# Kernel tuning notes

Hardware: AMD Instinct MI355X
Metric: run time of the kernel (lower is better)

## Reference

```python
import jax, jax.numpy as jnp
import numpy as np

B, SQ, SK, H, NH = 2, 2048, 2048, 1024, 16
HD = H // NH  # 64


def setup_inputs() -> dict:
    key = jax.random.key(0)
    ks = jax.random.split(key, 12)
    s = 1.0 / np.sqrt(H)
    inp = {
        "query": jax.random.normal(ks[0], (B, SQ, H), jnp.float32),
        "key": jax.random.normal(ks[1], (B, SK, H), jnp.float32),
        "value": jax.random.normal(ks[2], (B, SK, H), jnp.float32),
        # lower-triangular causal mask [B, SQ, SK]; nonzero = attend
        "causal_mask": jnp.broadcast_to(
            jnp.tril(jnp.ones((SQ, SK), jnp.int32)), (B, SQ, SK)
        ),
        "Wq": jax.random.uniform(ks[3], (H, H), jnp.float32, -s, s),
        "bq": jnp.zeros((H,), jnp.float32),
        "Wk": jax.random.uniform(ks[4], (H, H), jnp.float32, -s, s),
        "bk": jnp.zeros((H,), jnp.float32),
        "Wv": jax.random.uniform(ks[5], (H, H), jnp.float32, -s, s),
        "bv": jnp.zeros((H,), jnp.float32),
        "Wo": jax.random.uniform(ks[6], (H, H), jnp.float32, -s, s),
        "bo": jnp.zeros((H,), jnp.float32),
        "ln_g": jnp.ones((H,), jnp.float32),
        "ln_b": jnp.zeros((H,), jnp.float32),
    }
    return inp


def _layer_norm(x, g, b, eps=1e-5):
    mu = jnp.mean(x, axis=-1, keepdims=True)
    var = jnp.var(x, axis=-1, keepdims=True)
    return (x - mu) * jax.lax.rsqrt(var + eps) * g + b


def reference(query, key, value, causal_mask, Wq, bq, Wk, bk, Wv, bv, Wo, bo, ln_g, ln_b):
    # projections (torch Linear: x @ W.T + b)
    q = (query @ Wq.T + bq).reshape(B, SQ, NH, HD)
    k = (key @ Wk.T + bk).reshape(B, SK, NH, HD)
    v = (value @ Wv.T + bv).reshape(B, SK, NH, HD)
    # scores [B, NH, SQ, SK]
    scores = jnp.einsum("bqhd,bkhd->bhqk", q, k) / np.sqrt(HD).astype(np.float32)
    scores = jnp.where(causal_mask[:, None, :, :] == 0, -jnp.inf, scores)
    attn = jax.nn.softmax(scores, axis=-1)
    # dropout is identity in eval mode
    out = jnp.einsum("bhqk,bkhd->bqhd", attn, v).reshape(B, SQ, H)
    out = out @ Wo.T + bo
    return _layer_norm(query + out, ln_g, ln_b)
```

## Files before the change

kernel.cpp:

```cpp
#include <hip/hip_runtime.h>
#include <hip/hip_bf16.h>

#define SQL 2048
#define SKL 2048
#define HH  1024
#define NHH 16
#define HDD 64
#define BB  2
#define MM  (BB*SQL)

typedef __attribute__((ext_vector_type(8))) short short8;
typedef __attribute__((ext_vector_type(4))) short short4v;
typedef __attribute__((ext_vector_type(4))) float f32x4;
typedef unsigned short u16;

__device__ inline u16 f2bf(float f) {
    unsigned int u = __float_as_uint(f);
    u += 0x7fffu + ((u >> 16) & 1u);
    return (u16)(u >> 16);
}

__device__ inline void gl_lds16(const void* g, void* l) {
    __builtin_amdgcn_global_load_lds(
        (const __attribute__((address_space(1))) unsigned int*)g,
        (__attribute__((address_space(3))) unsigned int*)l, 16, 0, 0);
}

__global__ __launch_bounds__(256) void cvt_all_kernel(
    const float* __restrict__ q, const float* __restrict__ k, const float* __restrict__ v,
    const float* __restrict__ wq, const float* __restrict__ wk,
    const float* __restrict__ wv, const float* __restrict__ wo,
    u16* __restrict__ xq, u16* __restrict__ xk, u16* __restrict__ xv,
    u16* __restrict__ wqb, u16* __restrict__ wkb, u16* __restrict__ wvb, u16* __restrict__ wob)
{
    int b = blockIdx.x;
    const float* src; u16* dst;
    if      (b < 4096)  { src = q;  dst = xq; }
    else if (b < 8192)  { src = k;  dst = xk;  b -= 4096; }
    else if (b < 12288) { src = v;  dst = xv;  b -= 8192; }
    else if (b < 13312) { src = wq; dst = wqb; b -= 12288; }
    else if (b < 14336) { src = wk; dst = wkb; b -= 13312; }
    else if (b < 15360) { src = wv; dst = wvb; b -= 14336; }
    else                { src = wo; dst = wob; b -= 15360; }
    int i = (b * 256 + threadIdx.x) * 4;
    float4 vv = *(const float4*)(src + i);
    ushort4 oo;
    oo.x = f2bf(vv.x); oo.y = f2bf(vv.y); oo.z = f2bf(vv.z); oo.w = f2bf(vv.w);
    *(ushort4*)(dst + i) = oo;
}

template<int MODE>
__global__ __launch_bounds__(256) void gemm_kernel(
    const u16* __restrict__ A0, const u16* __restrict__ A1,
    const u16* __restrict__ W0, const u16* __restrict__ W1,
    const float* __restrict__ bias0, const float* __restrict__ bias1,
    u16* __restrict__ o0, u16* __restrict__ o1,
    const float* __restrict__ resid, float* __restrict__ outf)
{
    const int z = blockIdx.z;
    const u16* A = (MODE == 0 && z == 1) ? A1 : A0;
    const u16* W = (MODE == 0 && z == 1) ? W1 : W0;
    const float* bias = (MODE == 0 && z == 1) ? bias1 : bias0;
    u16* outb = (MODE == 0 && z == 1) ? o1 : o0;
    const float scale = (MODE == 0 && z == 0) ? 0.125f * 1.4426950408889634f : 1.0f;

    __shared__ u16 lds_a[128 * 32];
    __shared__ u16 lds_b[128 * 32];

    const int t = threadIdx.x;
    const int lane = t & 63;
    const int quad = lane >> 4;
    const int lo = lane & 15;
    const int wv = t >> 6;
    const int wm = (wv >> 1) * 64, wn = (wv & 1) * 64;
    const int m0 = blockIdx.x * 128;
    const int n0 = blockIdx.y * 128;

    f32x4 acc[4][4];
#pragma unroll
    for (int i = 0; i < 4; i++)
#pragma unroll
        for (int j = 0; j < 4; j++) acc[i][j] = (f32x4){0.f, 0.f, 0.f, 0.f};

    const int sl0 = t, sl1 = 256 + t;
    const int r0 = sl0 >> 2, c0 = ((sl0 & 3) ^ ((r0 >> 1) & 3)) * 8;
    const int r1 = sl1 >> 2, c1 = ((sl1 & 3) ^ ((r1 >> 1) & 3)) * 8;

    for (int k0 = 0; k0 < HH; k0 += 32) {
        gl_lds16(A + (size_t)(m0 + r0) * HH + k0 + c0, &lds_a[sl0 * 8]);
        gl_lds16(A + (size_t)(m0 + r1) * HH + k0 + c1, &lds_a[sl1 * 8]);
        gl_lds16(W + (size_t)(n0 + r0) * HH + k0 + c0, &lds_b[sl0 * 8]);
        gl_lds16(W + (size_t)(n0 + r1) * HH + k0 + c1, &lds_b[sl1 * 8]);
        __syncthreads();
        short8 af[4], bf[4];
#pragma unroll
        for (int i = 0; i < 4; i++) {
            const int ra = wm + i * 16 + lo;
            const int rb = wn + i * 16 + lo;
            af[i] = *(const short8*)&lds_a[ra * 32 + ((quad ^ ((ra >> 1) & 3)) * 8)];
            bf[i] = *(const short8*)&lds_b[rb * 32 + ((quad ^ ((rb >> 1) & 3)) * 8)];
        }
#pragma unroll
        for (int i = 0; i < 4; i++)
#pragma unroll
            for (int j = 0; j < 4; j++) {
                if (MODE == 2)
                    acc[i][j] = __builtin_amdgcn_mfma_f32_16x16x32_bf16(bf[j], af[i], acc[i][j], 0, 0, 0);
                else
                    acc[i][j] = __builtin_amdgcn_mfma_f32_16x16x32_bf16(af[i], bf[j], acc[i][j], 0, 0, 0);
            }
        __syncthreads();
    }

#pragma unroll
    for (int i = 0; i < 4; i++) {
#pragma unroll
        for (int j = 0; j < 4; j++) {
#pragma unroll
            for (int r = 0; r < 4; r++) {
                if (MODE == 2) {
                    int dg  = n0 + wn + j * 16 + quad * 4 + r;
                    int tok = m0 + wm + i * 16 + lo;
                    float val = acc[i][j][r] + bias[dg];
                    int head = dg >> 6, d = dg & 63;
                    int bi = tok >> 11, s = tok & 2047;
                    outb[(((size_t)bi * NHH + head) * HDD + d) * SKL + s] = f2bf(val);
                } else {
                    int row = m0 + wm + i * 16 + quad * 4 + r;
                    int col = n0 + wn + j * 16 + lo;
                    float val = acc[i][j][r] + bias[col];
                    if (MODE == 0) {
                        val *= scale;
                        int bi = row >> 11, s = row & 2047;
                        int head = col >> 6, d = col & 63;
                        outb[(((size_t)bi * NHH + head) * SQL + s) * HDD + d] = f2bf(val);
                    } else {
                        val += resid[(size_t)row * HH + col];
                        outf[(size_t)row * HH + col] = val;
                    }
                }
            }
        }
    }
}

#define PSTR 72

__global__ __launch_bounds__(256) void attn_kernel(
    const u16* __restrict__ qb, const u16* __restrict__ kb, const u16* __restrict__ vtb,
    u16* __restrict__ attn_out)
{
    __shared__ u16 k_lds[64 * 64];
    __shared__ u16 vt_lds[64 * 64];
    __shared__ u16 p_lds[4 * 16 * PSTR];

    const int t = threadIdx.x;
    const int lane = t & 63;
    const int quad = lane >> 4;
    const int lo = lane & 15;
    const int w = t >> 6;
    const int qt = (SQL / 64 - 1) - (blockIdx.x >> 5);
    const int bh = blockIdx.x & 31;
    const int q0 = qt * 64;

    const u16* qbase = qb + ((size_t)bh * SQL + q0 + w * 16 + lo) * HDD + quad * 8;
    short8 qf0 = *(const short8*)qbase;
    short8 qf1 = *(const short8*)(qbase + 32);

    float m_s = -__builtin_inff(), l_s = 0.f;
    f32x4 o[4];
#pragma unroll
    for (int j = 0; j < 4; j++) o[j] = (f32x4){0.f, 0.f, 0.f, 0.f};

    const int sl0 = t, sl1 = 256 + t;
    const int r0 = sl0 >> 3, c0 = ((sl0 & 7) ^ (r0 & 7)) * 8;
    const int r1 = sl1 >> 3, c1 = ((sl1 & 7) ^ (r1 & 7)) * 8;
    const u16* kbh = kb + (size_t)bh * SKL * HDD;
    const u16* vbh = vtb + (size_t)bh * HDD * SKL;
    u16* ppriv = &p_lds[w * 16 * PSTR];

    for (int kt = 0; kt <= qt; kt++) {
        const int k0 = kt * 64;
        gl_lds16(kbh + (size_t)(k0 + r0) * HDD + c0, &k_lds[sl0 * 8]);
        gl_lds16(kbh + (size_t)(k0 + r1) * HDD + c1, &k_lds[sl1 * 8]);
        gl_lds16(vbh + (size_t)r0 * SKL + k0 + c0, &vt_lds[sl0 * 8]);
        gl_lds16(vbh + (size_t)r1 * SKL + k0 + c1, &vt_lds[sl1 * 8]);
        __syncthreads();

        f32x4 s[4];
#pragma unroll
        for (int nt = 0; nt < 4; nt++) {
            const int row = nt * 16 + lo;
            short8 kf0 = *(const short8*)&k_lds[row * 64 + ((quad ^ (row & 7)) * 8)];
            short8 kf1 = *(const short8*)&k_lds[row * 64 + (((4 + quad) ^ (row & 7)) * 8)];
            s[nt] = (f32x4){0.f, 0.f, 0.f, 0.f};
            s[nt] = __builtin_amdgcn_mfma_f32_16x16x32_bf16(kf0, qf0, s[nt], 0, 0, 0);
            s[nt] = __builtin_amdgcn_mfma_f32_16x16x32_bf16(kf1, qf1, s[nt], 0, 0, 0);
        }
        if (kt == qt) {
            const int ql = w * 16 + lo;
#pragma unroll
            for (int nt = 0; nt < 4; nt++)
#pragma unroll
                for (int r = 0; r < 4; r++)
                    if (nt * 16 + quad * 4 + r > ql) s[nt][r] = -__builtin_inff();
        }

        float mx = s[0][0];
#pragma unroll
        for (int nt = 0; nt < 4; nt++)
#pragma unroll
            for (int r = 0; r < 4; r++) mx = fmaxf(mx, s[nt][r]);
        mx = fmaxf(mx, __shfl_xor(mx, 16));
        mx = fmaxf(mx, __shfl_xor(mx, 32));
        float mnew = fmaxf(m_s, mx);
        float al = __builtin_amdgcn_exp2f(m_s - mnew);
        m_s = mnew;
        float rs = 0.f;
#pragma unroll
        for (int nt = 0; nt < 4; nt++)
#pragma unroll
            for (int r = 0; r < 4; r++) {
                s[nt][r] = __builtin_amdgcn_exp2f(s[nt][r] - m_s);
                rs += s[nt][r];
            }
        rs += __shfl_xor(rs, 16);
        rs += __shfl_xor(rs, 32);
        l_s = l_s * al + rs;

        float alr[4];
#pragma unroll
        for (int r = 0; r < 4; r++) alr[r] = __shfl(al, quad * 4 + r, 16);
#pragma unroll
        for (int nt = 0; nt < 4; nt++)
#pragma unroll
            for (int r = 0; r < 4; r++) o[nt][r] *= alr[r];

#pragma unroll
        for (int nt = 0; nt < 4; nt++) {
            short4v pk;
#pragma unroll
            for (int r = 0; r < 4; r++) pk[r] = (short)f2bf(s[nt][r]);
            *(short4v*)&ppriv[lo * PSTR + nt * 16 + quad * 4] = pk;
        }
        short8 pf0 = *(const short8*)&ppriv[lo * PSTR + quad * 8];
        short8 pf1 = *(const short8*)&ppriv[lo * PSTR + 32 + quad * 8];

#pragma unroll
        for (int nt = 0; nt < 4; nt++) {
            const int row = nt * 16 + lo;
            short8 vf0 = *(const short8*)&vt_lds[row * 64 + ((quad ^ (row & 7)) * 8)];
            short8 vf1 = *(const short8*)&vt_lds[row * 64 + (((4 + quad) ^ (row & 7)) * 8)];
            o[nt] = __builtin_amdgcn_mfma_f32_16x16x32_bf16(pf0, vf0, o[nt], 0, 0, 0);
            o[nt] = __builtin_amdgcn_mfma_f32_16x16x32_bf16(pf1, vf1, o[nt], 0, 0, 0);
        }
        __syncthreads();
    }

    const int b = bh >> 4, h = bh & 15;
    float inv[4];
#pragma unroll
    for (int r = 0; r < 4; r++) inv[r] = 1.0f / __shfl(l_s, quad * 4 + r, 16);
#pragma unroll
    for (int nt = 0; nt < 4; nt++)
#pragma unroll
        for (int r = 0; r < 4; r++) {
            int srow = q0 + w * 16 + quad * 4 + r;
            attn_out[((size_t)b * SQL + srow) * HH + h * HDD + nt * 16 + lo] =
                f2bf(o[nt][r] * inv[r]);
        }
}

__global__ __launch_bounds__(256) void ln_kernel(const float* __restrict__ x,
                                                 const float* __restrict__ g,
                                                 const float* __restrict__ bb,
                                                 float* __restrict__ out)
{
    const int row = blockIdx.x;
    const int t = threadIdx.x;
    const float* xr = x + (size_t)row * HH;
    float4 v = *(const float4*)(xr + t * 4);
    float s1 = v.x + v.y + v.z + v.w;
    float s2 = v.x * v.x + v.y * v.y + v.z * v.z + v.w * v.w;
#pragma unroll
    for (int off = 32; off; off >>= 1) { s1 += __shfl_xor(s1, off); s2 += __shfl_xor(s2, off); }
    __shared__ float red[8];
    if ((t & 63) == 0) { red[(t >> 6) * 2] = s1; red[(t >> 6) * 2 + 1] = s2; }
    __syncthreads();
    s1 = red[0] + red[2] + red[4] + red[6];
    s2 = red[1] + red[3] + red[5] + red[7];
    float mu = s1 * (1.0f / HH);
    float var = s2 * (1.0f / HH) - mu * mu;
    float rstd = rsqrtf(var + 1e-5f);
    float4 gg = *(const float4*)(g + t * 4);
    float4 b4 = *(const float4*)(bb + t * 4);
    float4 o;
    o.x = (v.x - mu) * rstd * gg.x + b4.x;
    o.y = (v.y - mu) * rstd * gg.y + b4.y;
    o.z = (v.z - mu) * rstd * gg.z + b4.z;
    o.w = (v.w - mu) * rstd * gg.w + b4.w;
    *(float4*)(out + (size_t)row * HH + t * 4) = o;
}

extern "C" void kernel_launch(void* const* d_in, const int* in_sizes, int n_in,
                              void* d_out, int out_size, void* d_ws, size_t ws_size,
                              hipStream_t stream)
{
    const float* query = (const float*)d_in[0];
    const float* key   = (const float*)d_in[1];
    const float* value = (const float*)d_in[2];
    const float* Wq = (const float*)d_in[4];
    const float* bq = (const float*)d_in[5];
    const float* Wk = (const float*)d_in[6];
    const float* bk = (const float*)d_in[7];
    const float* Wv = (const float*)d_in[8];
    const float* bv = (const float*)d_in[9];
    const float* Wo = (const float*)d_in[10];
    const float* bo = (const float*)d_in[11];
    const float* ln_g = (const float*)d_in[12];
    const float* ln_b = (const float*)d_in[13];
    float* out = (float*)d_out;

    char* wp = (char*)d_ws;
    auto alloc = [&](size_t bytes) { void* p = (void*)wp; wp += (bytes + 255) & ~(size_t)255; return p; };
    const int nW = HH * HH;
    const int nX = MM * HH;
    u16* wqb = (u16*)alloc((size_t)nW * 2);
    u16* wkb = (u16*)alloc((size_t)nW * 2);
    u16* wvb = (u16*)alloc((size_t)nW * 2);
    u16* wob = (u16*)alloc((size_t)nW * 2);
    u16* xq  = (u16*)alloc((size_t)nX * 2);
    u16* xk  = (u16*)alloc((size_t)nX * 2);
    u16* xv  = (u16*)alloc((size_t)nX * 2);
    u16* qbuf = (u16*)alloc((size_t)nX * 2);
    u16* kbuf = (u16*)alloc((size_t)nX * 2);
    u16* vbuf = (u16*)alloc((size_t)nX * 2);
    u16* attnb = (u16*)alloc((size_t)nX * 2);
    float* projf = (float*)alloc((size_t)nX * 4);

    cvt_all_kernel<<<16384, 256, 0, stream>>>(query, key, value, Wq, Wk, Wv, Wo,
                                              xq, xk, xv, wqb, wkb, wvb, wob);

    gemm_kernel<0><<<dim3(32, 8, 2), 256, 0, stream>>>(
        xq, xk, wqb, wkb, bq, bk, qbuf, kbuf, nullptr, nullptr);
    gemm_kernel<2><<<dim3(32, 8, 1), 256, 0, stream>>>(
        xv, xv, wvb, wvb, bv, bv, vbuf, vbuf, nullptr, nullptr);

    attn_kernel<<<1024, 256, 0, stream>>>(qbuf, kbuf, vbuf, attnb);

    gemm_kernel<1><<<dim3(32, 8, 1), 256, 0, stream>>>(
        attnb, attnb, wob, wob, bo, bo, nullptr, nullptr, query, projf);

    ln_kernel<<<MM, 256, 0, stream>>>(projf, ln_g, ln_b, out);
}
```

Baseline: 264.9 us.

## Merge QKV projections into one launch, add lazy softmax rescale and packed bf16 converts

The Q/K and V projection GEMMs now run as a single three-slice launch, and the output projection gets its own dedicated kernel. In attention, rescaling of the running max is skipped unless the max grows by more than 8 in log2 space, which saves exp and multiply work on most tiles. The bf16 conversions now use the hardware packed-convert instruction, and MFMA sections are wrapped in s_setprio. The lazy rescale keeps a stale max, which risks larger exponent values, and the merged launch puts a runtime z branch inside the GEMM inner loop.

```diff
diff --git a/kernel.cpp b/kernel.cpp
--- a/kernel.cpp
+++ b/kernel.cpp
@@ -10,7 +10,6 @@
 #define MM  (BB*SQL)
 
 typedef __attribute__((ext_vector_type(8))) short short8;
-typedef __attribute__((ext_vector_type(4))) short short4v;
 typedef __attribute__((ext_vector_type(4))) float f32x4;
 typedef unsigned short u16;
 
@@ -18,6 +17,12 @@
     unsigned int u = __float_as_uint(f);
     u += 0x7fffu + ((u >> 16) & 1u);
     return (u16)(u >> 16);
+}
+
+__device__ inline unsigned int cvt_pk_bf16(float lo, float hi) {
+    unsigned int r;
+    asm("v_cvt_pk_bf16_f32 %0, %1, %2" : "=v"(r) : "v"(lo), "v"(hi));
+    return r;
 }
 
 __device__ inline void gl_lds16(const void* g, void* l) {
@@ -44,25 +49,23 @@
     else                { src = wo; dst = wob; b -= 15360; }
     int i = (b * 256 + threadIdx.x) * 4;
     float4 vv = *(const float4*)(src + i);
-    ushort4 oo;
-    oo.x = f2bf(vv.x); oo.y = f2bf(vv.y); oo.z = f2bf(vv.z); oo.w = f2bf(vv.w);
-    *(ushort4*)(dst + i) = oo;
-}
-
-template<int MODE>
-__global__ __launch_bounds__(256) void gemm_kernel(
-    const u16* __restrict__ A0, const u16* __restrict__ A1,
-    const u16* __restrict__ W0, const u16* __restrict__ W1,
-    const float* __restrict__ bias0, const float* __restrict__ bias1,
-    u16* __restrict__ o0, u16* __restrict__ o1,
-    const float* __restrict__ resid, float* __restrict__ outf)
+    unsigned int d0 = cvt_pk_bf16(vv.x, vv.y);
+    unsigned int d1 = cvt_pk_bf16(vv.z, vv.w);
+    *(uint2*)(dst + i) = make_uint2(d0, d1);
+}
+
+__global__ __launch_bounds__(256) void proj_kernel(
+    const u16* __restrict__ xq, const u16* __restrict__ xk, const u16* __restrict__ xv,
+    const u16* __restrict__ wqb, const u16* __restrict__ wkb, const u16* __restrict__ wvb,
+    const float* __restrict__ bq, const float* __restrict__ bk, const float* __restrict__ bv,
+    u16* __restrict__ oq, u16* __restrict__ ok, u16* __restrict__ ov)
 {
     const int z = blockIdx.z;
-    const u16* A = (MODE == 0 && z == 1) ? A1 : A0;
-    const u16* W = (MODE == 0 && z == 1) ? W1 : W0;
-    const float* bias = (MODE == 0 && z == 1) ? bias1 : bias0;
-    u16* outb = (MODE == 0 && z == 1) ? o1 : o0;
-    const float scale = (MODE == 0 && z == 0) ? 0.125f * 1.4426950408889634f : 1.0f;
+    const u16* A      = (z == 0) ? xq  : (z == 1) ? xk  : xv;
+    const u16* W      = (z == 0) ? wqb : (z == 1) ? wkb : wvb;
+    const float* bias = (z == 0) ? bq  : (z == 1) ? bk  : bv;
+    u16* outb         = (z == 0) ? oq  : (z == 1) ? ok  : ov;
+    const float scale = (z == 0) ? 0.125f * 1.4426950408889634f : 1.0f;
 
     __shared__ u16 lds_a[128 * 32];
     __shared__ u16 lds_b[128 * 32];
@@ -100,15 +103,19 @@
             af[i] = *(const short8*)&lds_a[ra * 32 + ((quad ^ ((ra >> 1) & 3)) * 8)];
             bf[i] = *(const short8*)&lds_b[rb * 32 + ((quad ^ ((rb >> 1) & 3)) * 8)];
         }
-#pragma unroll
-        for (int i = 0; i < 4; i++)
-#pragma unroll
-            for (int j = 0; j < 4; j++) {
-                if (MODE == 2)
+        if (z == 2) {
+#pragma unroll
+            for (int i = 0; i < 4; i++)
+#pragma unroll
+                for (int j = 0; j < 4; j++)
                     acc[i][j] = __builtin_amdgcn_mfma_f32_16x16x32_bf16(bf[j], af[i], acc[i][j], 0, 0, 0);
-                else
+        } else {
+#pragma unroll
+            for (int i = 0; i < 4; i++)
+#pragma unroll
+                for (int j = 0; j < 4; j++)
                     acc[i][j] = __builtin_amdgcn_mfma_f32_16x16x32_bf16(af[i], bf[j], acc[i][j], 0, 0, 0);
-            }
+        }
         __syncthreads();
     }
 
@@ -118,7 +125,7 @@
         for (int j = 0; j < 4; j++) {
 #pragma unroll
             for (int r = 0; r < 4; r++) {
-                if (MODE == 2) {
+                if (z == 2) {
                     int dg  = n0 + wn + j * 16 + quad * 4 + r;
                     int tok = m0 + wm + i * 16 + lo;
                     float val = acc[i][j][r] + bias[dg];
@@ -128,20 +135,76 @@
                 } else {
                     int row = m0 + wm + i * 16 + quad * 4 + r;
                     int col = n0 + wn + j * 16 + lo;
-                    float val = acc[i][j][r] + bias[col];
-                    if (MODE == 0) {
-                        val *= scale;
-                        int bi = row >> 11, s = row & 2047;
-                        int head = col >> 6, d = col & 63;
-                        outb[(((size_t)bi * NHH + head) * SQL + s) * HDD + d] = f2bf(val);
-                    } else {
-                        val += resid[(size_t)row * HH + col];
-                        outf[(size_t)row * HH + col] = val;
-                    }
+                    float val = (acc[i][j][r] + bias[col]) * scale;
+                    int bi = row >> 11, s = row & 2047;
+                    int head = col >> 6, d = col & 63;
+                    outb[(((size_t)bi * NHH + head) * SQL + s) * HDD + d] = f2bf(val);
                 }
             }
         }
     }
+}
+
+__global__ __launch_bounds__(256) void outproj_kernel(
+    const u16* __restrict__ A, const u16* __restrict__ W,
+    const float* __restrict__ bias, const float* __restrict__ resid,
+    float* __restrict__ outf)
+{
+    __shared__ u16 lds_a[128 * 32];
+    __shared__ u16 lds_b[128 * 32];
+
+    const int t = threadIdx.x;
+    const int lane = t & 63;
+    const int quad = lane >> 4;
+    const int lo = lane & 15;
+    const int wv = t >> 6;
+    const int wm = (wv >> 1) * 64, wn = (wv & 1) * 64;
+    const int m0 = blockIdx.x * 128;
+    const int n0 = blockIdx.y * 128;
+
+    f32x4 acc[4][4];
+#pragma unroll
+    for (int i = 0; i < 4; i++)
+#pragma unroll
+        for (int j = 0; j < 4; j++) acc[i][j] = (f32x4){0.f, 0.f, 0.f, 0.f};
+
+    const int sl0 = t, sl1 = 256 + t;
+    const int r0 = sl0 >> 2, c0 = ((sl0 & 3) ^ ((r0 >> 1) & 3)) * 8;
+    const int r1 = sl1 >> 2, c1 = ((sl1 & 3) ^ ((r1 >> 1) & 3)) * 8;
+
+    for (int k0 = 0; k0 < HH; k0 += 32) {
+        gl_lds16(A + (size_t)(m0 + r0) * HH + k0 + c0, &lds_a[sl0 * 8]);
+        gl_lds16(A + (size_t)(m0 + r1) * HH + k0 + c1, &lds_a[sl1 * 8]);
+        gl_lds16(W + (size_t)(n0 + r0) * HH + k0 + c0, &lds_b[sl0 * 8]);
+        gl_lds16(W + (size_t)(n0 + r1) * HH + k0 + c1, &lds_b[sl1 * 8]);
+        __syncthreads();
+        short8 af[4], bf[4];
+#pragma unroll
+        for (int i = 0; i < 4; i++) {
+            const int ra = wm + i * 16 + lo;
+            const int rb = wn + i * 16 + lo;
+            af[i] = *(const short8*)&lds_a[ra * 32 + ((quad ^ ((ra >> 1) & 3)) * 8)];
+            bf[i] = *(const short8*)&lds_b[rb * 32 + ((quad ^ ((rb >> 1) & 3)) * 8)];
+        }
+#pragma unroll
+        for (int i = 0; i < 4; i++)
+#pragma unroll
+            for (int j = 0; j < 4; j++)
+                acc[i][j] = __builtin_amdgcn_mfma_f32_16x16x32_bf16(af[i], bf[j], acc[i][j], 0, 0, 0);
+        __syncthreads();
+    }
+
+#pragma unroll
+    for (int i = 0; i < 4; i++)
+#pragma unroll
+        for (int j = 0; j < 4; j++)
+#pragma unroll
+            for (int r = 0; r < 4; r++) {
+                int row = m0 + wm + i * 16 + quad * 4 + r;
+                int col = n0 + wn + j * 16 + lo;
+                float val = acc[i][j][r] + bias[col] + resid[(size_t)row * HH + col];
+                outf[(size_t)row * HH + col] = val;
+            }
 }
 
 #define PSTR 72
@@ -188,6 +251,7 @@
         __syncthreads();
 
         f32x4 s[4];
+        __builtin_amdgcn_s_setprio(1);
 #pragma unroll
         for (int nt = 0; nt < 4; nt++) {
             const int row = nt * 16 + lo;
@@ -197,6 +261,7 @@
             s[nt] = __builtin_amdgcn_mfma_f32_16x16x32_bf16(kf0, qf0, s[nt], 0, 0, 0);
             s[nt] = __builtin_amdgcn_mfma_f32_16x16x32_bf16(kf1, qf1, s[nt], 0, 0, 0);
         }
+        __builtin_amdgcn_s_setprio(0);
         if (kt == qt) {
             const int ql = w * 16 + lo;
 #pragma unroll
@@ -213,9 +278,21 @@
             for (int r = 0; r < 4; r++) mx = fmaxf(mx, s[nt][r]);
         mx = fmaxf(mx, __shfl_xor(mx, 16));
         mx = fmaxf(mx, __shfl_xor(mx, 32));
-        float mnew = fmaxf(m_s, mx);
-        float al = __builtin_amdgcn_exp2f(m_s - mnew);
-        m_s = mnew;
+
+        if (!__all(mx - m_s <= 8.0f)) {
+            float mnew = fmaxf(m_s, mx);
+            float al = __builtin_amdgcn_exp2f(m_s - mnew);
+            m_s = mnew;
+            l_s *= al;
+            float alr[4];
+#pragma unroll
+            for (int r = 0; r < 4; r++) alr[r] = __shfl(al, quad * 4 + r, 16);
+#pragma unroll
+            for (int nt = 0; nt < 4; nt++)
+#pragma unroll
+                for (int r = 0; r < 4; r++) o[nt][r] *= alr[r];
+        }
+
         float rs = 0.f;
 #pragma unroll
         for (int nt = 0; nt < 4; nt++)
@@ -226,26 +303,18 @@
             }
         rs += __shfl_xor(rs, 16);
         rs += __shfl_xor(rs, 32);
-        l_s = l_s * al + rs;
-
-        float alr[4];
-#pragma unroll
-        for (int r = 0; r < 4; r++) alr[r] = __shfl(al, quad * 4 + r, 16);
-#pragma unroll
-        for (int nt = 0; nt < 4; nt++)
-#pragma unroll
-            for (int r = 0; r < 4; r++) o[nt][r] *= alr[r];
+        l_s += rs;
 
 #pragma unroll
         for (int nt = 0; nt < 4; nt++) {
-            short4v pk;
-#pragma unroll
-            for (int r = 0; r < 4; r++) pk[r] = (short)f2bf(s[nt][r]);
-            *(short4v*)&ppriv[lo * PSTR + nt * 16 + quad * 4] = pk;
+            unsigned int d0 = cvt_pk_bf16(s[nt][0], s[nt][1]);
+            unsigned int d1 = cvt_pk_bf16(s[nt][2], s[nt][3]);
+            *(uint2*)&ppriv[lo * PSTR + nt * 16 + quad * 4] = make_uint2(d0, d1);
         }
         short8 pf0 = *(const short8*)&ppriv[lo * PSTR + quad * 8];
         short8 pf1 = *(const short8*)&ppriv[lo * PSTR + 32 + quad * 8];
 
+        __builtin_amdgcn_s_setprio(1);
 #pragma unroll
         for (int nt = 0; nt < 4; nt++) {
             const int row = nt * 16 + lo;
@@ -254,6 +323,7 @@
             o[nt] = __builtin_amdgcn_mfma_f32_16x16x32_bf16(pf0, vf0, o[nt], 0, 0, 0);
             o[nt] = __builtin_amdgcn_mfma_f32_16x16x32_bf16(pf1, vf1, o[nt], 0, 0, 0);
         }
+        __builtin_amdgcn_s_setprio(0);
         __syncthreads();
     }
 
@@ -341,15 +411,12 @@
     cvt_all_kernel<<<16384, 256, 0, stream>>>(query, key, value, Wq, Wk, Wv, Wo,
                                               xq, xk, xv, wqb, wkb, wvb, wob);
 
-    gemm_kernel<0><<<dim3(32, 8, 2), 256, 0, stream>>>(
-        xq, xk, wqb, wkb, bq, bk, qbuf, kbuf, nullptr, nullptr);
-    gemm_kernel<2><<<dim3(32, 8, 1), 256, 0, stream>>>(
-        xv, xv, wvb, wvb, bv, bv, vbuf, vbuf, nullptr, nullptr);
+    proj_kernel<<<dim3(32, 8, 3), 256, 0, stream>>>(
+        xq, xk, xv, wqb, wkb, wvb, bq, bk, bv, qbuf, kbuf, vbuf);
 
     attn_kernel<<<1024, 256, 0, stream>>>(qbuf, kbuf, vbuf, attnb);
 
-    gemm_kernel<1><<<dim3(32, 8, 1), 256, 0, stream>>>(
-        attnb, attnb, wob, wob, bo, bo, nullptr, nullptr, query, projf);
+    outproj_kernel<<<dim3(32, 8), 256, 0, stream>>>(attnb, wob, bo, query, projf);
 
     ln_kernel<<<MM, 256, 0, stream>>>(projf, ln_g, ln_b, out);
 }
```

Measured after the change: 280.6 us. 1.06x slower.
